# Optimization experiments

Measured on AMD Instinct MI355X. Metric: run time of the kernel, lower is better.

Reference implementation:

```python
import jax, jax.numpy as jnp
import numpy as np

N_NODES = 128
N_EDGES = N_NODES * (N_NODES - 1)  # fully-connected, no self-loops
N_IN = 128
N_HID = 256
N_OUT = 128
BATCH = 32


def _build_rel_matrices():
    # one-hot incidence matrices for fully-connected off-diagonal graph
    send_idx, recv_idx = [], []
    for i in range(N_NODES):
        for j in range(N_NODES):
            if i != j:
                send_idx.append(i)
                recv_idx.append(j)
    eye = np.eye(N_NODES, dtype=np.float32)
    rel_send = eye[np.asarray(send_idx)]  # [E, N]
    rel_rec = eye[np.asarray(recv_idx)]   # [E, N]
    return jnp.asarray(rel_rec), jnp.asarray(rel_send)


def setup_inputs() -> dict:
    key = jax.random.key(0)
    k = jax.random.split(key, 6)
    rel_rec, rel_send = _build_rel_matrices()
    s1 = 1.0 / np.sqrt(2 * N_IN)
    s2 = 1.0 / np.sqrt(N_HID)
    return {
        "x": jax.random.normal(k[0], (BATCH, N_NODES, N_IN), dtype=jnp.float32),
        "rel_type": jax.random.uniform(k[1], (BATCH, N_EDGES, 4), dtype=jnp.float32),
        "rel_rec": rel_rec,
        "rel_send": rel_send,
        "W1": jax.random.normal(k[2], (2 * N_IN, N_HID), dtype=jnp.float32) * s1,
        "b1": jnp.zeros((N_HID,), dtype=jnp.float32),
        "W2": jax.random.normal(k[3], (N_HID, N_OUT), dtype=jnp.float32) * s2,
        "b2": jnp.zeros((N_OUT,), dtype=jnp.float32),
    }


def reference(x, rel_type, rel_rec, rel_send, W1, b1, W2, b2):
    # node2edge: gather sender/receiver node features via incidence matmuls
    senders = jnp.einsum('en,bnf->bef', rel_send, x)    # [B, E, n_in]
    receivers = jnp.einsum('en,bnf->bef', rel_rec, x)   # [B, E, n_in]
    edges = jnp.concatenate([senders, receivers], axis=-1)  # [B, E, 2*n_in]
    # 2-layer MLP on edges (rel_type is unused in the original forward)
    h = jax.nn.relu(edges @ W1 + b1)
    msg = h @ W2 + b2                                   # [B, E, n_out]
    # edge2node: scatter-sum then normalize by in-degree
    agg = jnp.einsum('en,bef->bnf', rel_rec, msg)       # [B, N, n_out]
    norm = rel_rec.sum(axis=0)[None, :, None]           # [1, N, 1]
    return agg / (norm + 1e-6)
```

## Files before the change

### kernel.cpp

```cpp
#include <hip/hip_runtime.h>

#define BATCH 32
#define NN    128
#define NIN   128
#define NHID  256
#define NOUT  128
#define ROWS  (BATCH * NN)

__global__ __launch_bounds__(256) void k1_sr(
    const float* __restrict__ x, const float* __restrict__ W1,
    const float* __restrict__ b1, float* __restrict__ S, float* __restrict__ R)
{
    __shared__ float xr[8][128];
    const int row0 = blockIdx.x * 8;
    const int t = threadIdx.x;
    for (int idx = t; idx < 8 * 128; idx += 256)
        xr[idx >> 7][idx & 127] = x[(size_t)row0 * NIN + idx];
    __syncthreads();

    const int c = t;
    float accs[8], accr[8];
#pragma unroll
    for (int r = 0; r < 8; ++r) { accs[r] = 0.f; accr[r] = 0.f; }

    for (int k = 0; k < NIN; k += 4) {
        float wa[4], wb[4];
#pragma unroll
        for (int kk = 0; kk < 4; ++kk) {
            wa[kk] = W1[(size_t)(k + kk) * NHID + c];
            wb[kk] = W1[(size_t)(NIN + k + kk) * NHID + c];
        }
#pragma unroll
        for (int r = 0; r < 8; ++r) {
            const float4 xv = *(const float4*)(&xr[r][k]);
            accs[r] = fmaf(xv.w, wa[3], fmaf(xv.z, wa[2], fmaf(xv.y, wa[1], fmaf(xv.x, wa[0], accs[r]))));
            accr[r] = fmaf(xv.w, wb[3], fmaf(xv.z, wb[2], fmaf(xv.y, wb[1], fmaf(xv.x, wb[0], accr[r]))));
        }
    }
    const float bias = b1[c];
#pragma unroll
    for (int r = 0; r < 8; ++r) {
        S[(size_t)(row0 + r) * NHID + c] = accs[r];
        R[(size_t)(row0 + r) * NHID + c] = accr[r] + bias;
    }
}

__global__ __launch_bounds__(512) void k2_fused(
    const float* __restrict__ S, const float* __restrict__ R,
    const float* __restrict__ W2, const float* __restrict__ b2,
    float* __restrict__ out)
{
    __shared__ float smem[128 * 256];

    const int blk = blockIdx.x;
    const int b   = blk >> 3;
    const int nt  = blk & 7;
    const int n0  = nt * 16;

    const int t = threadIdx.x;
    const int c = t & 255;
    const int h = t >> 8;

    const float4* Sv  = (const float4*)(S + (size_t)b * NN * NHID);
    float4*       sm4 = (float4*)smem;
#pragma unroll
    for (int it = 0; it < 16; ++it)
        sm4[t + it * 512] = Sv[t + it * 512];
    __syncthreads();

    const int r0 = n0 + h * 8;
    float rv[8], acc[8];
#pragma unroll
    for (int q = 0; q < 8; ++q) {
        rv[q]  = R[((size_t)(b * NN + r0 + q)) * NHID + c];
        acc[q] = 0.f;
    }

#pragma unroll 4
    for (int i = 0; i < NN; ++i) {
        const float s = smem[i * NHID + c];
#pragma unroll
        for (int q = 0; q < 8; ++q)
            acc[q] += fmaxf(s + rv[q], 0.f);
    }
#pragma unroll
    for (int q = 0; q < 8; ++q)
        acc[q] -= fmaxf(smem[(r0 + q) * NHID + c] + rv[q], 0.f);

    __syncthreads();
#pragma unroll
    for (int q = 0; q < 8; ++q)
        smem[(h * 8 + q) * NHID + c] = acc[q];
    __syncthreads();

    const int co = t & 127;
    const int rg = t >> 7;
    float acc3[4] = {0.f, 0.f, 0.f, 0.f};

    for (int k = 0; k < NHID; k += 4) {
        float w[4];
#pragma unroll
        for (int kk = 0; kk < 4; ++kk)
            w[kk] = W2[(size_t)(k + kk) * NOUT + co];
#pragma unroll
        for (int r = 0; r < 4; ++r) {
            const float4 gv = *(const float4*)(&smem[(rg * 4 + r) * NHID + k]);
            acc3[r] = fmaf(gv.w, w[3], fmaf(gv.z, w[2], fmaf(gv.y, w[1], fmaf(gv.x, w[0], acc3[r]))));
        }
    }
    const float inv  = 1.0f / (127.0f + 1e-6f);
    const float bias = 127.0f * b2[co];
#pragma unroll
    for (int r = 0; r < 4; ++r)
        out[((size_t)(b * NN + n0 + rg * 4 + r)) * NOUT + co] = (acc3[r] + bias) * inv;
}

extern "C" void kernel_launch(void* const* d_in, const int* in_sizes, int n_in,
                              void* d_out, int out_size, void* d_ws, size_t ws_size,
                              hipStream_t stream)
{
    const float* x  = (const float*)d_in[0];
    const float* W1 = (const float*)d_in[4];
    const float* b1 = (const float*)d_in[5];
    const float* W2 = (const float*)d_in[6];
    const float* b2 = (const float*)d_in[7];
    float* out = (float*)d_out;

    float* S = (float*)d_ws;
    float* R = S + (size_t)ROWS * NHID;

    k1_sr   <<<ROWS / 8,     256, 0, stream>>>(x, W1, b1, S, R);
    k2_fused<<<BATCH * 8,    512, 0, stream>>>(S, R, W2, b2, out);
}
```

Baseline: 116.0 us.

## Use packed f32x2 FMAs and relu-as-abs identity in edge aggregation

Both GEMM-like loops now use two-wide float vectors with elementwise fma so the compiler can emit packed FP32 instructions, splitting each accumulator into two partial sums that are added at the end. The relu-sum over senders is rewritten with relu(t) = 0.5*(t+|t|). The linear part collapses into a running sum of S plus 128*R, so the inner loop only does an add and an abs, both packable. The aim is to halve the VALU instruction count in the hot loops. In exchange the floating-point summation order changes slightly and register pressure may rise.

```diff
diff --git a/kernel.cpp b/kernel.cpp
--- a/kernel.cpp
+++ b/kernel.cpp
@@ -6,6 +6,8 @@
 #define NHID  256
 #define NOUT  128
 #define ROWS  (BATCH * NN)
+
+typedef __attribute__((ext_vector_type(2))) float f32x2;
 
 __global__ __launch_bounds__(256) void k1_sr(
     const float* __restrict__ x, const float* __restrict__ W1,
@@ -19,29 +21,32 @@
     __syncthreads();
 
     const int c = t;
-    float accs[8], accr[8];
+    f32x2 accs[8], accr[8];
 #pragma unroll
-    for (int r = 0; r < 8; ++r) { accs[r] = 0.f; accr[r] = 0.f; }
+    for (int r = 0; r < 8; ++r) { accs[r] = (f32x2)0.f; accr[r] = (f32x2)0.f; }
 
     for (int k = 0; k < NIN; k += 4) {
-        float wa[4], wb[4];
-#pragma unroll
-        for (int kk = 0; kk < 4; ++kk) {
-            wa[kk] = W1[(size_t)(k + kk) * NHID + c];
-            wb[kk] = W1[(size_t)(NIN + k + kk) * NHID + c];
-        }
+        f32x2 wa0, wa1, wb0, wb1;
+        wa0.x = W1[(size_t)(k+0)*NHID + c]; wa0.y = W1[(size_t)(k+1)*NHID + c];
+        wa1.x = W1[(size_t)(k+2)*NHID + c]; wa1.y = W1[(size_t)(k+3)*NHID + c];
+        wb0.x = W1[(size_t)(NIN+k+0)*NHID + c]; wb0.y = W1[(size_t)(NIN+k+1)*NHID + c];
+        wb1.x = W1[(size_t)(NIN+k+2)*NHID + c]; wb1.y = W1[(size_t)(NIN+k+3)*NHID + c];
 #pragma unroll
         for (int r = 0; r < 8; ++r) {
             const float4 xv = *(const float4*)(&xr[r][k]);
-            accs[r] = fmaf(xv.w, wa[3], fmaf(xv.z, wa[2], fmaf(xv.y, wa[1], fmaf(xv.x, wa[0], accs[r]))));
-            accr[r] = fmaf(xv.w, wb[3], fmaf(xv.z, wb[2], fmaf(xv.y, wb[1], fmaf(xv.x, wb[0], accr[r]))));
+            f32x2 xlo; xlo.x = xv.x; xlo.y = xv.y;
+            f32x2 xhi; xhi.x = xv.z; xhi.y = xv.w;
+            accs[r] = __builtin_elementwise_fma(xlo, wa0, accs[r]);
+            accs[r] = __builtin_elementwise_fma(xhi, wa1, accs[r]);
+            accr[r] = __builtin_elementwise_fma(xlo, wb0, accr[r]);
+            accr[r] = __builtin_elementwise_fma(xhi, wb1, accr[r]);
         }
     }
     const float bias = b1[c];
 #pragma unroll
     for (int r = 0; r < 8; ++r) {
-        S[(size_t)(row0 + r) * NHID + c] = accs[r];
-        R[(size_t)(row0 + r) * NHID + c] = accr[r] + bias;
+        S[(size_t)(row0 + r) * NHID + c] = accs[r].x + accs[r].y;
+        R[(size_t)(row0 + r) * NHID + c] = accr[r].x + accr[r].y + bias;
     }
 }
 
@@ -69,50 +74,71 @@
     __syncthreads();
 
     const int r0 = n0 + h * 8;
-    float rv[8], acc[8];
+    float rv[8];
 #pragma unroll
-    for (int q = 0; q < 8; ++q) {
-        rv[q]  = R[((size_t)(b * NN + r0 + q)) * NHID + c];
-        acc[q] = 0.f;
+    for (int q = 0; q < 8; ++q)
+        rv[q] = R[((size_t)(b * NN + r0 + q)) * NHID + c];
+
+    f32x2 rv2[4], aab[4];
+#pragma unroll
+    for (int j = 0; j < 4; ++j) {
+        rv2[j].x = rv[2*j]; rv2[j].y = rv[2*j+1];
+        aab[j] = (f32x2)0.f;
     }
+    float ssum = 0.f;
 
 #pragma unroll 4
     for (int i = 0; i < NN; ++i) {
         const float s = smem[i * NHID + c];
+        ssum += s;
+        f32x2 s2; s2.x = s; s2.y = s;
 #pragma unroll
-        for (int q = 0; q < 8; ++q)
-            acc[q] += fmaxf(s + rv[q], 0.f);
+        for (int j = 0; j < 4; ++j) {
+            const f32x2 tj = s2 + rv2[j];
+            aab[j].x += __builtin_fabsf(tj.x);
+            aab[j].y += __builtin_fabsf(tj.y);
+        }
     }
+
+    float gq[8];
 #pragma unroll
-    for (int q = 0; q < 8; ++q)
-        acc[q] -= fmaxf(smem[(r0 + q) * NHID + c] + rv[q], 0.f);
+    for (int q = 0; q < 8; ++q) {
+        const float aa   = (q & 1) ? aab[q >> 1].y : aab[q >> 1].x;
+        const float self = fmaxf(smem[(r0 + q) * NHID + c] + rv[q], 0.f);
+        gq[q] = 0.5f * (ssum + 128.f * rv[q] + aa) - self;
+    }
 
     __syncthreads();
 #pragma unroll
     for (int q = 0; q < 8; ++q)
-        smem[(h * 8 + q) * NHID + c] = acc[q];
+        smem[(h * 8 + q) * NHID + c] = gq[q];
     __syncthreads();
 
     const int co = t & 127;
     const int rg = t >> 7;
-    float acc3[4] = {0.f, 0.f, 0.f, 0.f};
+    f32x2 a2[4];
+#pragma unroll
+    for (int r = 0; r < 4; ++r) a2[r] = (f32x2)0.f;
 
     for (int k = 0; k < NHID; k += 4) {
-        float w[4];
-#pragma unroll
-        for (int kk = 0; kk < 4; ++kk)
-            w[kk] = W2[(size_t)(k + kk) * NOUT + co];
+        f32x2 w0, w1;
+        w0.x = W2[(size_t)(k+0)*NOUT + co]; w0.y = W2[(size_t)(k+1)*NOUT + co];
+        w1.x = W2[(size_t)(k+2)*NOUT + co]; w1.y = W2[(size_t)(k+3)*NOUT + co];
 #pragma unroll
         for (int r = 0; r < 4; ++r) {
             const float4 gv = *(const float4*)(&smem[(rg * 4 + r) * NHID + k]);
-            acc3[r] = fmaf(gv.w, w[3], fmaf(gv.z, w[2], fmaf(gv.y, w[1], fmaf(gv.x, w[0], acc3[r]))));
+            f32x2 glo; glo.x = gv.x; glo.y = gv.y;
+            f32x2 ghi; ghi.x = gv.z; ghi.y = gv.w;
+            a2[r] = __builtin_elementwise_fma(glo, w0, a2[r]);
+            a2[r] = __builtin_elementwise_fma(ghi, w1, a2[r]);
         }
     }
     const float inv  = 1.0f / (127.0f + 1e-6f);
     const float bias = 127.0f * b2[co];
 #pragma unroll
     for (int r = 0; r < 4; ++r)
-        out[((size_t)(b * NN + n0 + rg * 4 + r)) * NOUT + co] = (acc3[r] + bias) * inv;
+        out[((size_t)(b * NN + n0 + rg * 4 + r)) * NOUT + co] =
+            (a2[r].x + a2[r].y + bias) * inv;
 }
 
 extern "C" void kernel_launch(void* const* d_in, const int* in_sizes, int n_in,
@@ -129,6 +155,6 @@
     float* S = (float*)d_ws;
     float* R = S + (size_t)ROWS * NHID;
 
-    k1_sr   <<<ROWS / 8,     256, 0, stream>>>(x, W1, b1, S, R);
-    k2_fused<<<BATCH * 8,    512, 0, stream>>>(S, R, W2, b2, out);
+    k1_sr   <<<ROWS / 8,  256, 0, stream>>>(x, W1, b1, S, R);
+    k2_fused<<<BATCH * 8, 512, 0, stream>>>(S, R, W2, b2, out);
 }
```

New measurement: 116.4 us. Within noise of the previous version (+0.4%).
